# Performance work log

Measured on AMD Instinct MI355X. Metric: run time of the kernel, lower is better.

Reference implementation:

```python
import jax, jax.numpy as jnp
import numpy as np
import math

D_MODEL = 1024
FFN = 4096
NUM_HEAD = 16
HEAD_DIM = 64
BATCH = 4
SEQ = 2048
EPS = 1e-5


def _lin(k, out_dim, in_dim):
    bound = 1.0 / math.sqrt(in_dim)
    k1, k2 = jax.random.split(k)
    W = jax.random.uniform(k1, (out_dim, in_dim), jnp.float32, -bound, bound)
    b = jax.random.uniform(k2, (out_dim,), jnp.float32, -bound, bound)
    return W, b


def setup_inputs() -> dict:
    key = jax.random.key(0)
    ks = jax.random.split(key, 12)
    x = jax.random.normal(ks[0], (BATCH, SEQ, D_MODEL), jnp.float32)
    mask = jnp.zeros((SEQ, SEQ), jnp.float32)  # additive mask, broadcast over [H,B,S,S]
    Wq, bq = _lin(ks[1], D_MODEL, D_MODEL)
    Wk, bk = _lin(ks[2], D_MODEL, D_MODEL)
    Wv, bv = _lin(ks[3], D_MODEL, D_MODEL)
    Wo, bo = _lin(ks[4], D_MODEL, D_MODEL)
    gamma = jnp.ones((D_MODEL,), jnp.float32)
    beta = jnp.zeros((D_MODEL,), jnp.float32)
    W1, b1 = _lin(ks[5], FFN, D_MODEL)
    W2, b2 = _lin(ks[6], FFN // 2, FFN)
    W3, b3 = _lin(ks[7], FFN // 4, FFN // 2)
    W4, b4 = _lin(ks[8], D_MODEL, FFN // 4)
    Wl, bl = _lin(ks[9], D_MODEL, D_MODEL)
    return dict(x=x, mask=mask, Wq=Wq, bq=bq, Wk=Wk, bk=bk, Wv=Wv, bv=bv,
                Wo=Wo, bo=bo, gamma=gamma, beta=beta,
                W1=W1, b1=b1, W2=W2, b2=b2, W3=W3, b3=b3, W4=W4, b4=b4,
                Wl=Wl, bl=bl)


def _layernorm(x, gamma, beta):
    mean = jnp.mean(x, axis=-1, keepdims=True)
    var = jnp.mean((x - mean) ** 2, axis=-1, keepdims=True)
    return gamma * ((x - mean) / jnp.sqrt(var + EPS)) + beta


def _attention(x, mask, Wq, bq, Wk, bk, Wv, bv, Wo, bo):
    B, S, _ = x.shape
    def heads(W, b):
        return (x @ W.T + b).reshape(B, S, NUM_HEAD, HEAD_DIM).transpose(0, 2, 1, 3)
    q, k, v = heads(Wq, bq), heads(Wk, bk), heads(Wv, bv)  # [B,H,S,D]
    scaled = jnp.einsum('bhsd,bhtd->bhst', q, k) / math.sqrt(HEAD_DIM)
    # faithful to source: permute to [H,B,S,S], add mask, softmax, NaN->0,
    # then sum over dim=1 (which is BATCH here) -> [H,S,S]
    scaled = scaled.transpose(1, 0, 2, 3) + mask
    attn = jax.nn.softmax(scaled, axis=-1)
    attn = jnp.where(jnp.isnan(attn), 0.0, attn)
    A = jnp.sum(attn, axis=1)  # [H,S,S]
    V = jnp.einsum('hst,bhtd->bhsd', A, v)  # broadcast matmul as in torch
    V = V.transpose(0, 2, 1, 3).reshape(B, S, NUM_HEAD * HEAD_DIM)
    return V @ Wo.T + bo


def _ffn(x, W1, b1, W2, b2, W3, b3, W4, b4):
    x = jax.nn.relu(x @ W1.T + b1)
    x = jax.nn.relu(x @ W2.T + b2)
    x = jax.nn.relu(x @ W3.T + b3)
    return x @ W4.T + b4


def reference(x, mask, Wq, bq, Wk, bk, Wv, bv, Wo, bo, gamma, beta,
              W1, b1, W2, b2, W3, b3, W4, b4, Wl, bl):
    res = x
    x = _attention(x, mask, Wq, bq, Wk, bk, Wv, bv, Wo, bo)
    x = _layernorm(x + res, gamma, beta)
    res = x
    x = _ffn(x, W1, b1, W2, b2, W3, b3, W4, b4)
    x = _layernorm(res + x, gamma, beta)
    return x @ Wl.T + bl
```

## Files before the change

### kernel.cpp

```cpp
#include <hip/hip_runtime.h>
#include <stdint.h>

#define SEQL 2048
#define DM 1024
#define NH 16
#define DHD 64
#define NB 4
#define MT 8192

typedef __attribute__((ext_vector_type(8))) short bf16x8;
typedef __attribute__((ext_vector_type(4))) float f32x4;

__device__ __forceinline__ unsigned short f2bf(float f) {
  uint32_t u = __builtin_bit_cast(uint32_t, f);
  return (unsigned short)((u + 0x7FFFu + ((u >> 16) & 1u)) >> 16);
}
__device__ __forceinline__ float bf2f(unsigned short h) {
  return __builtin_bit_cast(float, (uint32_t)h << 16);
}
__device__ __forceinline__ float fexp2(float x) {
  float r;
  asm volatile("v_exp_f32 %0, %1" : "=v"(r) : "v"(x));
  return r;
}
__device__ __forceinline__ void glds16(const void* g, void* l) {
  __builtin_amdgcn_global_load_lds(
      (const __attribute__((address_space(1))) void*)g,
      (__attribute__((address_space(3))) void*)l, 16, 0, 0);
}
__device__ __forceinline__ void bar() {
  asm volatile("" ::: "memory");
  __builtin_amdgcn_s_barrier();
  asm volatile("" ::: "memory");
}
__device__ __forceinline__ void vm4() { asm volatile("s_waitcnt vmcnt(4)" ::: "memory"); }
__device__ __forceinline__ void vm0() { asm volatile("s_waitcnt vmcnt(0)" ::: "memory"); }

__global__ __launch_bounds__(256) void cast_f32_bf16(
    const float* __restrict__ in, unsigned short* __restrict__ out, int n8) {
  int i = blockIdx.x * 256 + threadIdx.x;
  if (i >= n8) return;
  const float4* p = (const float4*)(in + (size_t)i * 8);
  float4 a = p[0], b = p[1];
  uint32_t w0 = f2bf(a.x) | ((uint32_t)f2bf(a.y) << 16);
  uint32_t w1 = f2bf(a.z) | ((uint32_t)f2bf(a.w) << 16);
  uint32_t w2 = f2bf(b.x) | ((uint32_t)f2bf(b.y) << 16);
  uint32_t w3 = f2bf(b.z) | ((uint32_t)f2bf(b.w) << 16);
  int4 v = {(int)w0, (int)w1, (int)w2, (int)w3};
  *(int4*)(out + (size_t)i * 8) = v;
}


template <int MS, int NS, int MR, int MH>
__device__ __forceinline__ void mmaQ(f32x4 (&acc)[MR][4],
                                     const bf16x8 (&Ar)[MH][2],
                                     const bf16x8 (&Br)[2][2]) {
  __builtin_amdgcn_s_setprio(1);
#pragma unroll
  for (int m = 0; m < MH; m++)
#pragma unroll
    for (int n = 0; n < 2; n++)
#pragma unroll
      for (int kk = 0; kk < 2; kk++)
        acc[MS * MH + m][NS * 2 + n] = __builtin_amdgcn_mfma_f32_16x16x32_bf16(
            Ar[m][kk], Br[n][kk], acc[MS * MH + m][NS * 2 + n], 0, 0, 0);
  __builtin_amdgcn_s_setprio(0);
}

template <int MH>
__device__ __forceinline__ void loadF(bf16x8 (&Ar)[MH][2], const char* base,
                                      int row0, int g) {
#pragma unroll
  for (int m = 0; m < MH; m++) {
    int row = row0 + m * 16;
    int sw = (row & 7) << 4;
    Ar[m][0] = *(const bf16x8*)(base + row * 128 + ((g << 4) ^ sw));
    Ar[m][1] = *(const bf16x8*)(base + row * 128 + (((4 + g) << 4) ^ sw));
  }
}

template <int BM, bool RELU, int OMODE>
__global__ __launch_bounds__(512, 2) void gemm8(
    const unsigned short* __restrict__ Ag, const unsigned short* __restrict__ Bg,
    const float* __restrict__ bias0, const float* __restrict__ bias1,
    const float* __restrict__ bias2, void* C0, void* C1, void* C2, int N, int K,
    float sc0) {
  constexpr int MR = BM / 32;
  constexpr int MH = MR / 2;
  constexpr int AT = BM * 128;
  constexpr int BT = 256 * 128;
  __shared__ __align__(16) char lds[2 * AT + 2 * BT];
  char* Ab0 = lds;
  char* Ab1 = lds + AT;
  char* Bb0 = lds + 2 * AT;
  char* Bb1 = lds + 2 * AT + BT;

  const int tid = threadIdx.x;
  const int wid = tid >> 6, lane = tid & 63;
  const int wr = wid >> 2, wc = wid & 3;
  const int g = lane >> 4, ln = lane & 15;

  const int nbx = N >> 8;
  const int nwg = gridDim.x;
  const int cpx = nwg >> 3;
  const int wg = (blockIdx.x & 7) * cpx + (blockIdx.x >> 3);
  const int bm = wg / nbx, bn = wg % nbx;

  f32x4 acc[MR][4];
#pragma unroll
  for (int m = 0; m < MR; m++)
#pragma unroll
    for (int n = 0; n < 4; n++) acc[m][n] = (f32x4){0.f, 0.f, 0.f, 0.f};

  const int srow = wid * 8 + (lane >> 3);
  const int cs8 = ((lane & 7) ^ (lane >> 3)) * 8;
  const unsigned short* aBase = Ag + (size_t)(bm * BM + srow) * K + cs8;
  const unsigned short* bBase = Bg + (size_t)(bn * 256 + srow) * K + cs8;
  const int wofs = wid * 1024;

  auto stageA = [&](char* buf, int tt, int h) {
    const unsigned short* src = aBase + (size_t)(h * (BM / 2)) * K + tt * 64;
    char* dst = buf + h * (AT / 2) + wofs;
    glds16(src, dst);
    if constexpr (BM == 256) glds16(src + (size_t)64 * K, dst + 8192);
  };
  auto stageB = [&](char* buf, int tt, int h) {
    const unsigned short* src = bBase + (size_t)(h * 128) * K + tt * 64;
    char* dst = buf + h * (BT / 2) + wofs;
    glds16(src, dst);
    glds16(src + (size_t)64 * K, dst + 8192);
  };

  const int np = K >> 7;
  const int rowA0 = wr * (BM / 2) + ln;
  const int rowB0 = wc * 64 + ln;

  stageA(Ab0, 0, 0);
  stageA(Ab0, 0, 1);
  stageB(Bb0, 0, 0);
  stageB(Bb0, 0, 1);
  stageB(Bb1, 1, 0);
  stageB(Bb1, 1, 1);
  vm4();
  bar();

  bf16x8 Ar[MH][2], Br0[2][2], Br1[2][2];
  for (int i = 0; i < np; i++) {
    const int t = 2 * i;
    const bool sg = (i + 1 < np);
    loadF<MH>(Ar, Ab0, rowA0, g);
    loadF<2>(Br0, Bb0, rowB0, g);
    stageA(Ab1, t + 1, 0);
    bar();
    mmaQ<0, 0>(acc, Ar, Br0);
    bar();
    loadF<2>(Br1, Bb0, rowB0 + 32, g);
    stageA(Ab1, t + 1, 1);
    bar();
    mmaQ<0, 1>(acc, Ar, Br1);
    bar();
    loadF<MH>(Ar, Ab0, rowA0 + MH * 16, g);
    if (sg) stageB(Bb0, t + 2, 0);
    bar();
    mmaQ<1, 1>(acc, Ar, Br1);
    bar();
    if (sg) stageB(Bb0, t + 2, 1);
    bar();
    mmaQ<1, 0>(acc, Ar, Br0);
    if (sg) vm4(); else vm0();
    bar();
    loadF<MH>(Ar, Ab1, rowA0, g);
    loadF<2>(Br0, Bb1, rowB0, g);
    if (sg) stageA(Ab0, t + 2, 0);
    bar();
    mmaQ<0, 0>(acc, Ar, Br0);
    bar();
    loadF<2>(Br1, Bb1, rowB0 + 32, g);
    if (sg) stageA(Ab0, t + 2, 1);
    bar();
    mmaQ<0, 1>(acc, Ar, Br1);
    bar();
    loadF<MH>(Ar, Ab1, rowA0 + MH * 16, g);
    if (sg) stageB(Bb1, t + 3, 0);
    bar();
    mmaQ<1, 1>(acc, Ar, Br1);
    bar();
    if (sg) stageB(Bb1, t + 3, 1);
    bar();
    mmaQ<1, 0>(acc, Ar, Br0);
    if (sg) vm4();
    bar();
  }

  const int c0 = bn * 256 + wc * 64;
  const float* bias = bias0;
  float scl = sc0;
  unsigned short* outb = (unsigned short*)C0;
  float* outf = (float*)C0;
  int ldC = N;
  if constexpr (OMODE == 2) {
    int seg = bn >> 2;
    bias = seg == 0 ? bias0 : (seg == 1 ? bias1 : bias2);
    outb = (unsigned short*)(seg == 0 ? C0 : (seg == 1 ? C1 : C2));
    scl = seg == 0 ? sc0 : 1.0f;
    ldC = 1024;
  }
#pragma unroll
  for (int am = 0; am < MR; am++) {
#pragma unroll
    for (int n = 0; n < 4; n++) {
      int col = c0 + n * 16 + ln;
      int colL = (OMODE == 2) ? (col & 1023) : col;
      float bv = bias[colL];
#pragma unroll
      for (int r = 0; r < 4; r++) {
        int row = bm * BM + wr * (BM / 2) + am * 16 + g * 4 + r;
        float v = (acc[am][n][r] + bv) * scl;
        if constexpr (RELU) v = fmaxf(v, 0.f);
        if constexpr (OMODE == 0)
          outf[(size_t)row * ldC + colL] = v;
        else
          outb[(size_t)row * ldC + colL] = f2bf(v);
      }
    }
  }
}

__global__ __launch_bounds__(256) void attn_stats(
    const unsigned short* __restrict__ Q, const unsigned short* __restrict__ Kb,
    float* __restrict__ lst) {
  __shared__ unsigned short sK[64 * 64];
  const int blk = blockIdx.x;
  const int sblk = blk & 31;
  const int bh = blk >> 5;
  const int b = bh >> 4, h = bh & 15;
  const int tid = threadIdx.x;
  const int wid = tid >> 6, lane = tid & 63;
  const int g = lane >> 4;
  const int s0 = sblk * 64 + wid * 16;

  const unsigned short* qp =
      Q + (size_t)(b * SEQL + s0 + (lane & 15)) * DM + h * DHD + g * 8;
  bf16x8 q0 = *(const bf16x8*)qp;
  bf16x8 q1 = *(const bf16x8*)(qp + 32);

  const int srow = tid >> 3;
  const int sch = (tid & 7) ^ (srow & 7);
  const unsigned short* kg =
      Kb + (size_t)(b * SEQL + srow) * DM + h * DHD + sch * 8;
  char* l0 = (char*)sK + wid * 1024;
  char* l1 = (char*)sK + 4096 + wid * 1024;

  float lsum = 0.f;
  for (int t0 = 0; t0 < SEQL; t0 += 64) {
    __syncthreads();
    glds16(kg + (size_t)t0 * DM, l0);
    glds16(kg + (size_t)(t0 + 32) * DM, l1);
    __syncthreads();
#pragma unroll
    for (int tt = 0; tt < 4; tt++) {
      int row = tt * 16 + (lane & 15);
      const char* base = (const char*)sK + row * 128;
      bf16x8 k0 = *(const bf16x8*)(base + ((g ^ (row & 7)) * 16));
      bf16x8 k1 = *(const bf16x8*)(base + (((g + 4) ^ (row & 7)) * 16));
      f32x4 sc = {0.f, 0.f, 0.f, 0.f};
      sc = __builtin_amdgcn_mfma_f32_16x16x32_bf16(k0, q0, sc, 0, 0, 0);
      sc = __builtin_amdgcn_mfma_f32_16x16x32_bf16(k1, q1, sc, 0, 0, 0);
      lsum += fexp2(sc[0]) + fexp2(sc[1]) + fexp2(sc[2]) + fexp2(sc[3]);
    }
  }
  lsum += __shfl_xor(lsum, 16);
  lsum += __shfl_xor(lsum, 32);
  if (lane < 16) lst[(size_t)bh * SEQL + s0 + lane] = lsum;
}

__global__ __launch_bounds__(256) void attn_apply(
    const unsigned short* __restrict__ Q, const unsigned short* __restrict__ Kb,
    const unsigned short* __restrict__ Vb, const float* __restrict__ lst,
    unsigned short* __restrict__ ctx) {
  __shared__ unsigned short sK[4][32 * 64];
  __shared__ unsigned short v_lds[4][64][40];
  __shared__ unsigned short a_lds[4][16][40];
  const int blk = blockIdx.x;
  const int sblk = blk & 31;
  const int h = blk >> 5;
  const int tid = threadIdx.x;
  const int wid = tid >> 6, lane = tid & 63;
  const int g = lane >> 4;
  const int s0 = sblk * 64 + wid * 16;

  bf16x8 q[4][2];
#pragma unroll
  for (int b = 0; b < 4; b++) {
    const unsigned short* qp =
        Q + (size_t)(b * SEQL + s0 + (lane & 15)) * DM + h * DHD + g * 8;
    q[b][0] = *(const bf16x8*)qp;
    q[b][1] = *(const bf16x8*)(qp + 32);
  }
  float rl[4];
#pragma unroll
  for (int b = 0; b < 4; b++)
    rl[b] = 1.0f / lst[(size_t)(b * NH + h) * SEQL + s0 + (lane & 15)];

  f32x4 o[4][4];
#pragma unroll
  for (int b = 0; b < 4; b++)
#pragma unroll
    for (int c = 0; c < 4; c++) o[b][c] = (f32x4){0.f, 0.f, 0.f, 0.f};

  const int krow = tid >> 3;
  const int kch = (tid & 7) ^ (krow & 7);
  const int vt = lane >> 1;
  const int vd0 = (lane & 1) * 32;
  const unsigned short* vp0 =
      Vb + (size_t)(wid * SEQL + vt) * DM + h * DHD + vd0;

  for (int t0 = 0; t0 < SEQL; t0 += 32) {
    int4 vv[4];
#pragma unroll
    for (int q4 = 0; q4 < 4; q4++)
      vv[q4] = *(const int4*)(vp0 + (size_t)t0 * DM + q4 * 8);
    __syncthreads();
#pragma unroll
    for (int q4 = 0; q4 < 4; q4++) {
      uint32_t ws[4] = {(uint32_t)vv[q4].x, (uint32_t)vv[q4].y,
                        (uint32_t)vv[q4].z, (uint32_t)vv[q4].w};
#pragma unroll
      for (int w2 = 0; w2 < 4; w2++) {
        v_lds[wid][vd0 + q4 * 8 + w2 * 2][vt] = (unsigned short)ws[w2];
        v_lds[wid][vd0 + q4 * 8 + w2 * 2 + 1][vt] = (unsigned short)(ws[w2] >> 16);
      }
    }
#pragma unroll
    for (int b = 0; b < 4; b++)
      glds16(Kb + (size_t)(b * SEQL + t0 + krow) * DM + h * DHD + kch * 8,
             (char*)&sK[b][0] + wid * 1024);
    __syncthreads();

    float at[2][4];
#pragma unroll
    for (int tt = 0; tt < 2; tt++)
#pragma unroll
      for (int r = 0; r < 4; r++) at[tt][r] = 0.f;
#pragma unroll
    for (int b = 0; b < 4; b++) {
#pragma unroll
      for (int tt = 0; tt < 2; tt++) {
        int row = tt * 16 + (lane & 15);
        const char* base = (const char*)&sK[b][0] + row * 128;
        bf16x8 k0 = *(const bf16x8*)(base + ((g ^ (row & 7)) * 16));
        bf16x8 k1 = *(const bf16x8*)(base + (((g + 4) ^ (row & 7)) * 16));
        f32x4 sc = {0.f, 0.f, 0.f, 0.f};
        sc = __builtin_amdgcn_mfma_f32_16x16x32_bf16(k0, q[b][0], sc, 0, 0, 0);
        sc = __builtin_amdgcn_mfma_f32_16x16x32_bf16(k1, q[b][1], sc, 0, 0, 0);
#pragma unroll
        for (int r = 0; r < 4; r++)
          at[tt][r] = fmaf(fexp2(sc[r]), rl[b], at[tt][r]);
      }
    }
#pragma unroll
    for (int tt = 0; tt < 2; tt++)
#pragma unroll
      for (int r = 0; r < 4; r++)
        a_lds[wid][lane & 15][tt * 16 + g * 4 + r] = f2bf(at[tt][r]);
    bf16x8 af = *(const bf16x8*)&a_lds[wid][lane & 15][g * 8];
#pragma unroll
    for (int b = 0; b < 4; b++)
#pragma unroll
      for (int c = 0; c < 4; c++) {
        bf16x8 bv = *(const bf16x8*)&v_lds[b][c * 16 + (lane & 15)][g * 8];
        o[b][c] = __builtin_amdgcn_mfma_f32_16x16x32_bf16(af, bv, o[b][c], 0, 0, 0);
      }
  }

#pragma unroll
  for (int b = 0; b < 4; b++)
#pragma unroll
    for (int c = 0; c < 4; c++)
#pragma unroll
      for (int r = 0; r < 4; r++) {
        int srow = s0 + g * 4 + r;
        size_t off = (size_t)(b * SEQL + srow) * DM + h * DHD + c * 16 + (lane & 15);
        ctx[off] = f2bf(o[b][c][r]);
      }
}

template <bool RESBF16>
__global__ __launch_bounds__(256) void ln_kernel(
    const float* __restrict__ a, const void* __restrict__ res,
    const float* __restrict__ gamma, const float* __restrict__ beta,
    unsigned short* __restrict__ obf) {
  __shared__ float red[8];
  const int row = blockIdx.x;
  const int tid = threadIdx.x;
  const size_t base = (size_t)row * DM + tid * 4;
  float4 va = *(const float4*)(a + base);
  float v0, v1, v2, v3;
  if (RESBF16) {
    const unsigned short* rp = (const unsigned short*)res + base;
    ushort4 u = *(const ushort4*)rp;
    v0 = va.x + bf2f(u.x);
    v1 = va.y + bf2f(u.y);
    v2 = va.z + bf2f(u.z);
    v3 = va.w + bf2f(u.w);
  } else {
    float4 vr = *(const float4*)((const float*)res + base);
    v0 = va.x + vr.x;
    v1 = va.y + vr.y;
    v2 = va.z + vr.z;
    v3 = va.w + vr.w;
  }
  float sum = v0 + v1 + v2 + v3;
#pragma unroll
  for (int off = 1; off < 64; off <<= 1) sum += __shfl_xor(sum, off);
  const int wid = tid >> 6, lane = tid & 63;
  if (lane == 0) red[wid] = sum;
  __syncthreads();
  float mean = (red[0] + red[1] + red[2] + red[3]) * (1.0f / DM);
  float d0 = v0 - mean, d1 = v1 - mean, d2 = v2 - mean, d3 = v3 - mean;
  float sq = d0 * d0 + d1 * d1 + d2 * d2 + d3 * d3;
#pragma unroll
  for (int off = 1; off < 64; off <<= 1) sq += __shfl_xor(sq, off);
  if (lane == 0) red[4 + wid] = sq;
  __syncthreads();
  float var = (red[4] + red[5] + red[6] + red[7]) * (1.0f / DM);
  float rstd = rsqrtf(var + 1e-5f);
  float4 gm = *(const float4*)(gamma + tid * 4);
  float4 bb = *(const float4*)(beta + tid * 4);
  float o0 = gm.x * (d0 * rstd) + bb.x;
  float o1 = gm.y * (d1 * rstd) + bb.y;
  float o2 = gm.z * (d2 * rstd) + bb.z;
  float o3 = gm.w * (d3 * rstd) + bb.w;
  uint32_t w0 = f2bf(o0) | ((uint32_t)f2bf(o1) << 16);
  uint32_t w1 = f2bf(o2) | ((uint32_t)f2bf(o3) << 16);
  uint2 pk = {w0, w1};
  *(uint2*)(obf + base) = pk;
}

extern "C" void kernel_launch(void* const* d_in, const int* in_sizes, int n_in,
                              void* d_out, int out_size, void* d_ws, size_t ws_size,
                              hipStream_t stream) {
  (void)in_sizes; (void)n_in; (void)out_size; (void)ws_size;
  const float* x  = (const float*)d_in[0];
  const float* Wq = (const float*)d_in[2];  const float* bq = (const float*)d_in[3];
  const float* Wk = (const float*)d_in[4];  const float* bk = (const float*)d_in[5];
  const float* Wv = (const float*)d_in[6];  const float* bv = (const float*)d_in[7];
  const float* Wo = (const float*)d_in[8];  const float* bo = (const float*)d_in[9];
  const float* gamma = (const float*)d_in[10]; const float* beta = (const float*)d_in[11];
  const float* W1 = (const float*)d_in[12]; const float* b1 = (const float*)d_in[13];
  const float* W2 = (const float*)d_in[14]; const float* b2 = (const float*)d_in[15];
  const float* W3 = (const float*)d_in[16]; const float* b3 = (const float*)d_in[17];
  const float* W4 = (const float*)d_in[18]; const float* b4 = (const float*)d_in[19];
  const float* Wl = (const float*)d_in[20]; const float* bl = (const float*)d_in[21];
  float* out = (float*)d_out;

  char* w = (char*)d_ws;
  const size_t MB = 1024 * 1024;
  unsigned short* xb   = (unsigned short*)(w);
  unsigned short* Qb   = (unsigned short*)(w + 16 * MB);
  unsigned short* Kbf  = (unsigned short*)(w + 32 * MB);
  unsigned short* Vbf  = (unsigned short*)(w + 48 * MB);
  float* lst = (float*)(w + 64 * MB);
  unsigned short* ctx  = (unsigned short*)(w + 65 * MB);
  unsigned short* wbuf = (unsigned short*)(w + 81 * MB);
  float* aproj = (float*)(w + 97 * MB);
  unsigned short* ln1b = (unsigned short*)(w + 129 * MB);
  unsigned short* h1   = (unsigned short*)(w);
  unsigned short* h2   = (unsigned short*)(w + 97 * MB);
  unsigned short* h3   = (unsigned short*)(w + 65 * MB);
  float* ffo  = (float*)(w);
  unsigned short* ln2b = (unsigned short*)(w + 32 * MB);

  auto cast = [&](const float* src, unsigned short* dst, size_t n) {
    int n8 = (int)(n / 8);
    cast_f32_bf16<<<dim3((n8 + 255) / 256), dim3(256), 0, stream>>>(src, dst, n8);
  };
  const float QSCALE = 0.125f * 1.44269504088896f;

  cast(x, xb, (size_t)MT * DM);
  cast(Wq, wbuf, (size_t)DM * DM);
  cast(Wk, wbuf + (size_t)DM * DM, (size_t)DM * DM);
  cast(Wv, wbuf + (size_t)2 * DM * DM, (size_t)DM * DM);
  gemm8<256, false, 2><<<dim3((MT / 256) * (3072 / 256)), dim3(512), 0, stream>>>(
      xb, wbuf, bq, bk, bv, Qb, Kbf, Vbf, 3072, 1024, QSCALE);
  attn_stats<<<dim3(NB * NH * (SEQL / 64)), dim3(256), 0, stream>>>(Qb, Kbf, lst);
  attn_apply<<<dim3(NH * (SEQL / 64)), dim3(256), 0, stream>>>(Qb, Kbf, Vbf, lst, ctx);
  cast(Wo, wbuf, (size_t)DM * DM);
  gemm8<128, false, 0><<<dim3((MT / 128) * 4), dim3(512), 0, stream>>>(
      ctx, wbuf, bo, nullptr, nullptr, aproj, nullptr, nullptr, 1024, 1024, 1.0f);
  ln_kernel<false><<<dim3(MT), dim3(256), 0, stream>>>(aproj, x, gamma, beta, ln1b);
  cast(W1, wbuf, (size_t)4096 * DM);
  gemm8<256, true, 1><<<dim3((MT / 256) * 16), dim3(512), 0, stream>>>(
      ln1b, wbuf, b1, nullptr, nullptr, h1, nullptr, nullptr, 4096, 1024, 1.0f);
  cast(W2, wbuf, (size_t)2048 * 4096);
  gemm8<256, true, 1><<<dim3((MT / 256) * 8), dim3(512), 0, stream>>>(
      h1, wbuf, b2, nullptr, nullptr, h2, nullptr, nullptr, 2048, 4096, 1.0f);
  cast(W3, wbuf, (size_t)1024 * 2048);
  gemm8<128, true, 1><<<dim3((MT / 128) * 4), dim3(512), 0, stream>>>(
      h2, wbuf, b3, nullptr, nullptr, h3, nullptr, nullptr, 1024, 2048, 1.0f);
  cast(W4, wbuf, (size_t)DM * DM);
  gemm8<128, false, 0><<<dim3((MT / 128) * 4), dim3(512), 0, stream>>>(
      h3, wbuf, b4, nullptr, nullptr, ffo, nullptr, nullptr, 1024, 1024, 1.0f);
  ln_kernel<true><<<dim3(MT), dim3(256), 0, stream>>>(ffo, ln1b, gamma, beta, ln2b);
  cast(Wl, wbuf, (size_t)DM * DM);
  gemm8<128, false, 0><<<dim3((MT / 128) * 4), dim3(512), 0, stream>>>(
      ln2b, wbuf, bl, nullptr, nullptr, out, nullptr, nullptr, 1024, 1024, 1.0f);
}
```

Baseline: 659.9 us.

## Split attention apply over key halves and pre-transpose V for async LDS loads

Adds a V-transpose kernel so attn_apply can stream V tiles into shared memory with direct global-to-LDS loads, replacing the per-element scatter transpose in the inner loop. It also splits the key dimension in two, doubling the grid from 512 to 1024 blocks for better occupancy on the many-CU device. The two partial outputs are summed by a new bf16 add kernel. This adds an extra V pass, an extra output pass, and a second bf16 rounding of partial sums.

```diff
diff --git a/kernel.cpp b/kernel.cpp
--- a/kernel.cpp
+++ b/kernel.cpp
@@ -50,6 +50,52 @@
   *(int4*)(out + (size_t)i * 8) = v;
 }
 
+__global__ __launch_bounds__(256) void addb(
+    const unsigned short* __restrict__ a, unsigned short* __restrict__ bio, int n8) {
+  int i = blockIdx.x * 256 + threadIdx.x;
+  if (i >= n8) return;
+  int4 va = *(const int4*)(a + (size_t)i * 8);
+  int4 vb = *(const int4*)(bio + (size_t)i * 8);
+  uint32_t* pa = (uint32_t*)&va;
+  uint32_t* pb = (uint32_t*)&vb;
+  int4 vo;
+  uint32_t* po = (uint32_t*)&vo;
+#pragma unroll
+  for (int j = 0; j < 4; j++) {
+    float lo = bf2f((unsigned short)pa[j]) + bf2f((unsigned short)pb[j]);
+    float hi = bf2f((unsigned short)(pa[j] >> 16)) + bf2f((unsigned short)(pb[j] >> 16));
+    po[j] = f2bf(lo) | ((uint32_t)f2bf(hi) << 16);
+  }
+  *(int4*)(bio + (size_t)i * 8) = vo;
+}
+
+__global__ __launch_bounds__(256) void vtrans(
+    const unsigned short* __restrict__ V, unsigned short* __restrict__ Vt) {
+  __shared__ unsigned short td[64][72];
+  const int blk = blockIdx.x;
+  const int t64 = blk & 31;
+  const int b = (blk >> 5) & 3;
+  const int h = blk >> 7;
+  const int tid = threadIdx.x;
+  const int r = tid >> 3, c8 = (tid & 7) * 8;
+  const unsigned short* src = V + (size_t)(b * SEQL + t64 * 64) * DM + h * 64;
+#pragma unroll
+  for (int half = 0; half < 2; half++) {
+    int4 v = *(const int4*)(src + (size_t)(r + half * 32) * DM + c8);
+    *(int4*)&td[r + half * 32][c8] = v;
+  }
+  __syncthreads();
+  unsigned short* dst = Vt + (size_t)((h * 4 + b) * 64) * SEQL + t64 * 64;
+#pragma unroll
+  for (int half = 0; half < 2; half++) {
+    int tk = tid + half * 256;
+    int d = tk >> 3, tc = (tk & 7) * 8;
+    unsigned short tmp[8];
+#pragma unroll
+    for (int j = 0; j < 8; j++) tmp[j] = td[tc + j][d];
+    *(int4*)(dst + (size_t)d * SEQL + tc) = *(int4*)tmp;
+  }
+}
 
 template <int MS, int NS, int MR, int MH>
 __device__ __forceinline__ void mmaQ(f32x4 (&acc)[MR][4],
@@ -276,31 +322,33 @@
 
 __global__ __launch_bounds__(256) void attn_apply(
     const unsigned short* __restrict__ Q, const unsigned short* __restrict__ Kb,
-    const unsigned short* __restrict__ Vb, const float* __restrict__ lst,
-    unsigned short* __restrict__ ctx) {
+    const unsigned short* __restrict__ Vt, const float* __restrict__ lst,
+    unsigned short* __restrict__ op0, unsigned short* __restrict__ op1) {
   __shared__ unsigned short sK[4][32 * 64];
-  __shared__ unsigned short v_lds[4][64][40];
+  __shared__ unsigned short vT[4][64 * 32];
   __shared__ unsigned short a_lds[4][16][40];
   const int blk = blockIdx.x;
-  const int sblk = blk & 31;
-  const int h = blk >> 5;
+  const int tpart = blk & 1;
+  const int sblk = (blk >> 1) & 31;
+  const int h = blk >> 6;
   const int tid = threadIdx.x;
   const int wid = tid >> 6, lane = tid & 63;
-  const int g = lane >> 4;
+  const int g = lane >> 4, ln = lane & 15;
   const int s0 = sblk * 64 + wid * 16;
+  const int tbase = tpart * (SEQL / 2);
 
   bf16x8 q[4][2];
 #pragma unroll
   for (int b = 0; b < 4; b++) {
     const unsigned short* qp =
-        Q + (size_t)(b * SEQL + s0 + (lane & 15)) * DM + h * DHD + g * 8;
+        Q + (size_t)(b * SEQL + s0 + ln) * DM + h * DHD + g * 8;
     q[b][0] = *(const bf16x8*)qp;
     q[b][1] = *(const bf16x8*)(qp + 32);
   }
   float rl[4];
 #pragma unroll
   for (int b = 0; b < 4; b++)
-    rl[b] = 1.0f / lst[(size_t)(b * NH + h) * SEQL + s0 + (lane & 15)];
+    rl[b] = 1.0f / lst[(size_t)(b * NH + h) * SEQL + s0 + ln];
 
   f32x4 o[4][4];
 #pragma unroll
@@ -310,31 +358,19 @@
 
   const int krow = tid >> 3;
   const int kch = (tid & 7) ^ (krow & 7);
-  const int vt = lane >> 1;
-  const int vd0 = (lane & 1) * 32;
-  const unsigned short* vp0 =
-      Vb + (size_t)(wid * SEQL + vt) * DM + h * DHD + vd0;
-
-  for (int t0 = 0; t0 < SEQL; t0 += 32) {
-    int4 vv[4];
-#pragma unroll
-    for (int q4 = 0; q4 < 4; q4++)
-      vv[q4] = *(const int4*)(vp0 + (size_t)t0 * DM + q4 * 8);
+  const unsigned short* vsrc =
+      Vt + (size_t)((h * 4 + wid) * 64 + (lane >> 2)) * SEQL + (lane & 3) * 8;
+
+  for (int t0 = tbase; t0 < tbase + SEQL / 2; t0 += 32) {
     __syncthreads();
-#pragma unroll
-    for (int q4 = 0; q4 < 4; q4++) {
-      uint32_t ws[4] = {(uint32_t)vv[q4].x, (uint32_t)vv[q4].y,
-                        (uint32_t)vv[q4].z, (uint32_t)vv[q4].w};
-#pragma unroll
-      for (int w2 = 0; w2 < 4; w2++) {
-        v_lds[wid][vd0 + q4 * 8 + w2 * 2][vt] = (unsigned short)ws[w2];
-        v_lds[wid][vd0 + q4 * 8 + w2 * 2 + 1][vt] = (unsigned short)(ws[w2] >> 16);
-      }
-    }
 #pragma unroll
     for (int b = 0; b < 4; b++)
       glds16(Kb + (size_t)(b * SEQL + t0 + krow) * DM + h * DHD + kch * 8,
-             (char*)&sK[b][0] + wid * 1024);
+             (char*)sK + b * 4096 + wid * 1024);
+#pragma unroll
+    for (int qq = 0; qq < 4; qq++)
+      glds16(vsrc + (size_t)(qq * 16) * SEQL + t0,
+             (char*)vT + wid * 4096 + qq * 1024);
     __syncthreads();
 
     float at[2][4];
@@ -346,8 +382,8 @@
     for (int b = 0; b < 4; b++) {
 #pragma unroll
       for (int tt = 0; tt < 2; tt++) {
-        int row = tt * 16 + (lane & 15);
-        const char* base = (const char*)&sK[b][0] + row * 128;
+        int row = tt * 16 + ln;
+        const char* base = (const char*)sK + b * 4096 + row * 128;
         bf16x8 k0 = *(const bf16x8*)(base + ((g ^ (row & 7)) * 16));
         bf16x8 k1 = *(const bf16x8*)(base + (((g + 4) ^ (row & 7)) * 16));
         f32x4 sc = {0.f, 0.f, 0.f, 0.f};
@@ -362,17 +398,19 @@
     for (int tt = 0; tt < 2; tt++)
 #pragma unroll
       for (int r = 0; r < 4; r++)
-        a_lds[wid][lane & 15][tt * 16 + g * 4 + r] = f2bf(at[tt][r]);
-    bf16x8 af = *(const bf16x8*)&a_lds[wid][lane & 15][g * 8];
+        a_lds[wid][ln][tt * 16 + g * 4 + r] = f2bf(at[tt][r]);
+    bf16x8 af = *(const bf16x8*)&a_lds[wid][ln][g * 8];
 #pragma unroll
     for (int b = 0; b < 4; b++)
 #pragma unroll
       for (int c = 0; c < 4; c++) {
-        bf16x8 bv = *(const bf16x8*)&v_lds[b][c * 16 + (lane & 15)][g * 8];
+        bf16x8 bv =
+            *(const bf16x8*)((const char*)vT + b * 4096 + (c * 16 + ln) * 64 + g * 16);
         o[b][c] = __builtin_amdgcn_mfma_f32_16x16x32_bf16(af, bv, o[b][c], 0, 0, 0);
       }
   }
 
+  unsigned short* op = tpart ? op1 : op0;
 #pragma unroll
   for (int b = 0; b < 4; b++)
 #pragma unroll
@@ -380,8 +418,8 @@
 #pragma unroll
       for (int r = 0; r < 4; r++) {
         int srow = s0 + g * 4 + r;
-        size_t off = (size_t)(b * SEQL + srow) * DM + h * DHD + c * 16 + (lane & 15);
-        ctx[off] = f2bf(o[b][c][r]);
+        size_t off = (size_t)(b * SEQL + srow) * DM + h * DHD + c * 16 + ln;
+        op[off] = f2bf(o[b][c][r]);
       }
 }
 
@@ -465,6 +503,9 @@
   unsigned short* wbuf = (unsigned short*)(w + 81 * MB);
   float* aproj = (float*)(w + 97 * MB);
   unsigned short* ln1b = (unsigned short*)(w + 129 * MB);
+  unsigned short* Vt   = (unsigned short*)(w + 97 * MB);
+  unsigned short* op0  = (unsigned short*)(w);
+  unsigned short* op1  = ctx;
   unsigned short* h1   = (unsigned short*)(w);
   unsigned short* h2   = (unsigned short*)(w + 97 * MB);
   unsigned short* h3   = (unsigned short*)(w + 65 * MB);
@@ -483,8 +524,10 @@
   cast(Wv, wbuf + (size_t)2 * DM * DM, (size_t)DM * DM);
   gemm8<256, false, 2><<<dim3((MT / 256) * (3072 / 256)), dim3(512), 0, stream>>>(
       xb, wbuf, bq, bk, bv, Qb, Kbf, Vbf, 3072, 1024, QSCALE);
+  vtrans<<<dim3(NH * NB * (SEQL / 64)), dim3(256), 0, stream>>>(Vbf, Vt);
   attn_stats<<<dim3(NB * NH * (SEQL / 64)), dim3(256), 0, stream>>>(Qb, Kbf, lst);
-  attn_apply<<<dim3(NH * (SEQL / 64)), dim3(256), 0, stream>>>(Qb, Kbf, Vbf, lst, ctx);
+  attn_apply<<<dim3(NH * 32 * 2), dim3(256), 0, stream>>>(Qb, Kbf, Vt, lst, op0, op1);
+  addb<<<dim3((MT * DM / 8 + 255) / 256), dim3(256), 0, stream>>>(op0, ctx, MT * DM / 8);
   cast(Wo, wbuf, (size_t)DM * DM);
   gemm8<128, false, 0><<<dim3((MT / 128) * 4), dim3(512), 0, stream>>>(
       ctx, wbuf, bo, nullptr, nullptr, aproj, nullptr, nullptr, 1024, 1024, 1.0f);
```

Result: no change. 652.4 us (-1.1%).
